# Performance work log

Measured on AMD Instinct MI355X. Metric: run time of the kernel, lower is better.

## Reference

```python
import jax, jax.numpy as jnp
import numpy as np

B, N, F, H = 1024, 64, 512, 512  # batch, n_agents, input_size, hidden


def setup_inputs() -> dict:
    key = jax.random.key(0)
    k1, k2, k3, k4, k5, k6 = jax.random.split(key, 6)
    locs = jax.random.uniform(k1, (B, N, 2), dtype=jnp.float32)
    states = jax.random.normal(k2, (B, N, F), dtype=jnp.float32)
    # CatEdgeGraphLayer: Linear(2*F + 2 -> H)
    Wg = jax.random.normal(k3, (H, 2 * F + 2), dtype=jnp.float32) / np.sqrt(2 * F + 2)
    bg = jnp.zeros((H,), dtype=jnp.float32)
    W4 = jax.random.normal(k4, (2, H), dtype=jnp.float32) / np.sqrt(H)
    b4 = jnp.zeros((2,), dtype=jnp.float32)
    W5 = jax.random.normal(k5, (1, H), dtype=jnp.float32) / np.sqrt(H)
    b5 = jnp.zeros((1,), dtype=jnp.float32)
    return {"locs": locs, "states": states, "Wg": Wg, "bg": bg,
            "W4": W4, "b4": b4, "W5": W5, "b5": b5}


def _forward(locs, states, Wg, bg, W4, b4, W5, b5):
    n = states.shape[1]
    f = states.shape[2]
    # get_diffs: pairwise position differences d[b,i,j] = locs[b,i] - locs[b,j]
    diffs = locs[:, :, None, :] - locs[:, None, :, :]          # [B,N,N,2]
    norms = jnp.linalg.norm(diffs, axis=-1)                    # [B,N,N]
    # threshold = ||normalize([1,1])|| = 1.0
    threshold = jnp.float32(1.0)
    A = (norms < threshold).astype(states.dtype)
    # normalize_adjacency: row-normalize (diagonal is 1 so rows never empty)
    A = A / jnp.sum(A, axis=-1, keepdims=True)
    # message j->i (j != i): A[b,i,j] * concat(states[b,j], diffs[b,i,j])
    Am = A * (1.0 - jnp.eye(n, dtype=A.dtype))                 # mask j == i
    # per-agent update: relu( sum_{j!=i} Linear(concat(f_i, msg_ij)) )
    # split weight by input blocks: W1 acts on f_i, W2f on f_j part, W2d on diff part
    W1, W2f, W2d = Wg[:, :f], Wg[:, f:2 * f], Wg[:, 2 * f:]
    msg_f = jnp.einsum('bij,bjf->bif', Am, states)             # sum_j A_ij f_j
    msg_d = jnp.einsum('bij,bijc->bic', Am, diffs)             # sum_j A_ij d_ij
    pre = ((n - 1) * (jnp.einsum('bif,hf->bih', states, W1) + bg)
           + jnp.einsum('bif,hf->bih', msg_f, W2f)
           + jnp.einsum('bic,hc->bih', msg_d, W2d))
    h = jax.nn.relu(pre)                                       # [B,N,H]
    policies = jnp.einsum('bih,ph->bip', h, W4) + b4           # [B,N,2]
    values = jnp.einsum('bih,vh->biv', h, W5) + b5             # [B,N,1]
    return policies, values


def reference(locs, states, Wg, bg, W4, b4, W5, b5):
    return _forward(locs, states, Wg, bg, W4, b4, W5, b5)
```

## Files before the change

### kernel.cpp

```cpp
#include <hip/hip_runtime.h>


typedef __attribute__((ext_vector_type(8))) short bf16x8;
typedef __attribute__((ext_vector_type(4))) float f32x4;
typedef __attribute__((ext_vector_type(4))) unsigned short us4;

__device__ __forceinline__ unsigned short f2bf(float x) {
  union { float f; unsigned int u; } c; c.f = x;
  return (unsigned short)((c.u + 0x7FFFu + ((c.u >> 16) & 1u)) >> 16);
}

__global__ void prep_kernel(const float* __restrict__ Wg, const float* __restrict__ bg,
                            const float* __restrict__ W4, const float* __restrict__ W5,
                            unsigned short* __restrict__ Wgb, float* __restrict__ auxw)
{
  const int h = blockIdx.x;
  const int t = threadIdx.x;
  const float* row = Wg + h * 1026;
  const int k0 = t * 4;
#pragma unroll
  for (int q = 0; q < 4; ++q) {
    int k = k0 + q;
    float s = (k < 512) ? 63.0f : 1.0f;
    Wgb[h * 1024 + k] = f2bf(s * row[k]);
  }
  if (t == 0) {
    float* a = auxw + h * 8;
    a[0] = 63.0f * bg[h];
    a[1] = row[1024];
    a[2] = row[1025];
    a[3] = W4[h];
    a[4] = W4[512 + h];
    a[5] = W5[h];
    a[6] = 0.0f; a[7] = 0.0f;
  }
}

__global__ __launch_bounds__(256, 1) void traffic_kernel(
    const float* __restrict__ locs, const float* __restrict__ states,
    const unsigned short* __restrict__ Wgb, const float* __restrict__ auxw,
    const float* __restrict__ b4, const float* __restrict__ b5,
    float* __restrict__ out)
{
  __shared__ unsigned short S[64 * 520];
  __shared__ unsigned short U2T[512 * 72];
  __shared__ unsigned short Am[64 * 72];
  __shared__ float locs_s[128];
  __shared__ float msgd[128];
  __shared__ float red[4 * 64 * 3];

  const int t = threadIdx.x;
  const int b = blockIdx.x;
  const int lane = t & 63;
  const int w = t >> 6;
  const int llo = lane & 15;
  const int lhi = lane >> 4;

  if (t < 128) locs_s[t] = locs[b * 128 + t];
  __syncthreads();

  {
    const int i = t >> 2;
    const int j0 = (t & 3) * 16;
    const float xi = locs_s[2*i], yi = locs_s[2*i+1];
    float a[16]; float psum = 0.f;
#pragma unroll
    for (int q = 0; q < 16; ++q) {
      int j = j0 + q;
      float dx = xi - locs_s[2*j];
      float dy = yi - locs_s[2*j+1];
      a[q] = (dx*dx + dy*dy < 1.0f) ? 1.0f : 0.0f;
      psum += a[q];
    }
    psum += __shfl_xor(psum, 1);
    psum += __shfl_xor(psum, 2);
    const float inv = 1.0f / psum;
    float m0 = 0.f, m1 = 0.f;
#pragma unroll
    for (int q = 0; q < 16; ++q) {
      int j = j0 + q;
      float v = (j == i) ? 0.f : a[q] * inv;
      a[q] = v;
      m0 += v * (xi - locs_s[2*j]);
      m1 += v * (yi - locs_s[2*j+1]);
    }
    m0 += __shfl_xor(m0, 1); m0 += __shfl_xor(m0, 2);
    m1 += __shfl_xor(m1, 1); m1 += __shfl_xor(m1, 2);
    if ((t & 3) == 0) { msgd[2*i] = m0; msgd[2*i+1] = m1; }
    union { unsigned short h8[8]; uint4 v4; } pk;
#pragma unroll
    for (int q = 0; q < 8; ++q) pk.h8[q] = f2bf(a[q]);
    *(uint4*)&Am[i*72 + j0] = pk.v4;
#pragma unroll
    for (int q = 0; q < 8; ++q) pk.h8[q] = f2bf(a[8+q]);
    *(uint4*)&Am[i*72 + j0 + 8] = pk.v4;
  }

  {
    const float4* sb = (const float4*)(states + (size_t)b * 32768);
#pragma unroll
    for (int it = 0; it < 32; ++it) {
      int id = it * 256 + t;
      int j = id >> 7;
      int f0 = (id & 127) * 4;
      float4 v = sb[id];
      us4 s4;
      s4.x = f2bf(v.x); s4.y = f2bf(v.y);
      s4.z = f2bf(v.z); s4.w = f2bf(v.w);
      *(us4*)&S[j * 520 + f0] = s4;
    }
  }
  __syncthreads();

  const int hw = w * 128;
  unsigned short* U2w = &U2T[w * 128 * 72];

  f32x4 acc[8][4];

  auto zero_acc = [&]() {
#pragma unroll
    for (int mt = 0; mt < 8; ++mt)
#pragma unroll
      for (int nt = 0; nt < 4; ++nt)
        acc[mt][nt] = f32x4{0.f, 0.f, 0.f, 0.f};
  };

  auto gemm_step = [&](int kg, int kl) {
    bf16x8 afr[8], bfr[4];
#pragma unroll
    for (int mt = 0; mt < 8; ++mt)
      afr[mt] = *(const bf16x8*)&Wgb[(size_t)(hw + mt*16 + llo) * 1024 + kg + lhi*8];
#pragma unroll
    for (int nt = 0; nt < 4; ++nt)
      bfr[nt] = *(const bf16x8*)&S[(nt*16 + llo) * 520 + kl + lhi*8];
#pragma unroll
    for (int mt = 0; mt < 8; ++mt)
#pragma unroll
      for (int nt = 0; nt < 4; ++nt)
        acc[mt][nt] = __builtin_amdgcn_mfma_f32_16x16x32_bf16(afr[mt], bfr[nt], acc[mt][nt], 0, 0, 0);
  };

  zero_acc();
#pragma unroll 2
  for (int ks = 0; ks < 16; ++ks) gemm_step(512 + ks*32, ks*32);

#pragma unroll
  for (int mt = 0; mt < 8; ++mt)
#pragma unroll
    for (int nt = 0; nt < 4; ++nt)
#pragma unroll
      for (int r = 0; r < 4; ++r)
        U2w[(mt*16 + lhi*4 + r) * 72 + nt*16 + llo] = f2bf(acc[mt][nt][r]);

  zero_acc();
#pragma unroll 2
  for (int ks = 0; ks < 16; ++ks) gemm_step(ks*32, ks*32);

#pragma unroll
  for (int ks = 0; ks < 2; ++ks) {
    bf16x8 afr[8], bfr[4];
#pragma unroll
    for (int mt = 0; mt < 8; ++mt)
      afr[mt] = *(const bf16x8*)&U2w[(mt*16 + llo) * 72 + ks*32 + lhi*8];
#pragma unroll
    for (int nt = 0; nt < 4; ++nt)
      bfr[nt] = *(const bf16x8*)&Am[(nt*16 + llo) * 72 + ks*32 + lhi*8];
#pragma unroll
    for (int mt = 0; mt < 8; ++mt)
#pragma unroll
      for (int nt = 0; nt < 4; ++nt)
        acc[mt][nt] = __builtin_amdgcn_mfma_f32_16x16x32_bf16(afr[mt], bfr[nt], acc[mt][nt], 0, 0, 0);
  }

  float mdx[4], mdy[4];
#pragma unroll
  for (int nt = 0; nt < 4; ++nt) {
    mdx[nt] = msgd[2*(nt*16 + llo)];
    mdy[nt] = msgd[2*(nt*16 + llo) + 1];
  }
  float pp0[4] = {0,0,0,0}, pp1[4] = {0,0,0,0}, vv[4] = {0,0,0,0};
#pragma unroll
  for (int mt = 0; mt < 8; ++mt) {
#pragma unroll
    for (int r = 0; r < 4; ++r) {
      int hh = hw + mt*16 + lhi*4 + r;
      float4 ax0 = *(const float4*)&auxw[hh*8];
      float4 ax1 = *(const float4*)&auxw[hh*8 + 4];
#pragma unroll
      for (int nt = 0; nt < 4; ++nt) {
        float val = acc[mt][nt][r] + ax0.x + mdx[nt]*ax0.y + mdy[nt]*ax0.z;
        val = fmaxf(val, 0.f);
        pp0[nt] += val * ax0.w;
        pp1[nt] += val * ax1.x;
        vv[nt]  += val * ax1.y;
      }
    }
  }
#pragma unroll
  for (int nt = 0; nt < 4; ++nt) {
    pp0[nt] += __shfl_xor(pp0[nt], 16); pp0[nt] += __shfl_xor(pp0[nt], 32);
    pp1[nt] += __shfl_xor(pp1[nt], 16); pp1[nt] += __shfl_xor(pp1[nt], 32);
    vv[nt]  += __shfl_xor(vv[nt], 16);  vv[nt]  += __shfl_xor(vv[nt], 32);
  }
  if (lane < 16) {
#pragma unroll
    for (int nt = 0; nt < 4; ++nt) {
      int i = nt*16 + llo;
      red[(w*64 + i)*3 + 0] = pp0[nt];
      red[(w*64 + i)*3 + 1] = pp1[nt];
      red[(w*64 + i)*3 + 2] = vv[nt];
    }
  }
  __syncthreads();
  if (t < 192) {
    int o = t >> 6;
    int i = t & 63;
    float s = red[(0*64+i)*3+o] + red[(1*64+i)*3+o]
            + red[(2*64+i)*3+o] + red[(3*64+i)*3+o];
    s += (o < 2) ? b4[o] : b5[0];
    if (o < 2) out[((size_t)b*64 + i)*2 + o] = s;
    else       out[(size_t)131072 + (size_t)b*64 + i] = s;
  }
}

extern "C" void kernel_launch(void* const* d_in, const int* in_sizes, int n_in,
                              void* d_out, int out_size, void* d_ws, size_t ws_size,
                              hipStream_t stream)
{
  const float* locs   = (const float*)d_in[0];
  const float* states = (const float*)d_in[1];
  const float* Wg     = (const float*)d_in[2];
  const float* bg     = (const float*)d_in[3];
  const float* W4     = (const float*)d_in[4];
  const float* b4     = (const float*)d_in[5];
  const float* W5     = (const float*)d_in[6];
  const float* b5     = (const float*)d_in[7];

  unsigned short* Wgb = (unsigned short*)d_ws;
  float* auxw = (float*)((char*)d_ws + 512 * 1024 * 2);

  prep_kernel<<<512, 256, 0, stream>>>(Wg, bg, W4, W5, Wgb, auxw);
  traffic_kernel<<<1024, 256, 0, stream>>>(locs, states, Wgb, auxw, b4, b5, (float*)d_out);
}
```

Measured before the change: 408.4 us.

## Halve LDS footprint by staging states in halves to fit two blocks per CU

The main kernel now stages the bf16 states tile in two 32-agent halves and drops the large U2T shared buffer. The W2f·S product is instead transposed through a small per-wave scratch into register A-fragments that feed the adjacency MFMA directly. This cuts shared memory enough to allow two blocks per CU (launch_bounds 256,2), aiming at better latency hiding, at the cost of an extra barrier and tighter register pressure. The prep kernel is also reshaped to write packed bf16 pairs, one pair per thread.

```diff
diff --git a/kernel.cpp b/kernel.cpp
--- a/kernel.cpp
+++ b/kernel.cpp
@@ -10,21 +10,21 @@
   return (unsigned short)((c.u + 0x7FFFu + ((c.u >> 16) & 1u)) >> 16);
 }
 
-__global__ void prep_kernel(const float* __restrict__ Wg, const float* __restrict__ bg,
-                            const float* __restrict__ W4, const float* __restrict__ W5,
-                            unsigned short* __restrict__ Wgb, float* __restrict__ auxw)
+__global__ __launch_bounds__(256) void prep_kernel(
+    const float* __restrict__ Wg, const float* __restrict__ bg,
+    const float* __restrict__ W4, const float* __restrict__ W5,
+    unsigned short* __restrict__ Wgb, float* __restrict__ auxw)
 {
-  const int h = blockIdx.x;
-  const int t = threadIdx.x;
+  const int id = blockIdx.x * 256 + threadIdx.x;
+  const int h = id >> 9;
+  const int kp = id & 511;
+  const int k = kp * 2;
   const float* row = Wg + h * 1026;
-  const int k0 = t * 4;
-#pragma unroll
-  for (int q = 0; q < 4; ++q) {
-    int k = k0 + q;
-    float s = (k < 512) ? 63.0f : 1.0f;
-    Wgb[h * 1024 + k] = f2bf(s * row[k]);
-  }
-  if (t == 0) {
+  const float s = (k < 512) ? 63.0f : 1.0f;
+  unsigned int lo = f2bf(s * row[k]);
+  unsigned int hi = f2bf(s * row[k + 1]);
+  *(unsigned int*)&Wgb[h * 1024 + k] = lo | (hi << 16);
+  if (kp == 0) {
     float* a = auxw + h * 8;
     a[0] = 63.0f * bg[h];
     a[1] = row[1024];
@@ -36,15 +36,15 @@
   }
 }
 
-__global__ __launch_bounds__(256, 1) void traffic_kernel(
+__global__ __launch_bounds__(256, 2) void traffic_kernel(
     const float* __restrict__ locs, const float* __restrict__ states,
     const unsigned short* __restrict__ Wgb, const float* __restrict__ auxw,
     const float* __restrict__ b4, const float* __restrict__ b5,
     float* __restrict__ out)
 {
-  __shared__ unsigned short S[64 * 520];
-  __shared__ unsigned short U2T[512 * 72];
+  __shared__ unsigned short S[32 * 520];
   __shared__ unsigned short Am[64 * 72];
+  __shared__ unsigned short scr[4][16 * 40];
   __shared__ float locs_s[128];
   __shared__ float msgd[128];
   __shared__ float red[4 * 64 * 3];
@@ -55,6 +55,7 @@
   const int w = t >> 6;
   const int llo = lane & 15;
   const int lhi = lane >> 4;
+  const int hw = w * 128;
 
   if (t < 128) locs_s[t] = locs[b * 128 + t];
   __syncthreads();
@@ -96,10 +97,10 @@
     *(uint4*)&Am[i*72 + j0 + 8] = pk.v4;
   }
 
-  {
-    const float4* sb = (const float4*)(states + (size_t)b * 32768);
-#pragma unroll
-    for (int it = 0; it < 32; ++it) {
+  auto stageS = [&](int half) {
+    const float4* sb = (const float4*)(states + (size_t)b * 32768 + half * 16384);
+#pragma unroll
+    for (int it = 0; it < 16; ++it) {
       int id = it * 256 + t;
       int j = id >> 7;
       int f0 = (id & 127) * 4;
@@ -109,68 +110,89 @@
       s4.z = f2bf(v.z); s4.w = f2bf(v.w);
       *(us4*)&S[j * 520 + f0] = s4;
     }
-  }
-  __syncthreads();
-
-  const int hw = w * 128;
-  unsigned short* U2w = &U2T[w * 128 * 72];
+  };
 
   f32x4 acc[8][4];
-
-  auto zero_acc = [&]() {
-#pragma unroll
-    for (int mt = 0; mt < 8; ++mt)
-#pragma unroll
-      for (int nt = 0; nt < 4; ++nt)
-        acc[mt][nt] = f32x4{0.f, 0.f, 0.f, 0.f};
-  };
-
-  auto gemm_step = [&](int kg, int kl) {
-    bf16x8 afr[8], bfr[4];
-#pragma unroll
-    for (int mt = 0; mt < 8; ++mt)
-      afr[mt] = *(const bf16x8*)&Wgb[(size_t)(hw + mt*16 + llo) * 1024 + kg + lhi*8];
-#pragma unroll
-    for (int nt = 0; nt < 4; ++nt)
-      bfr[nt] = *(const bf16x8*)&S[(nt*16 + llo) * 520 + kl + lhi*8];
-#pragma unroll
-    for (int mt = 0; mt < 8; ++mt)
-#pragma unroll
-      for (int nt = 0; nt < 4; ++nt)
-        acc[mt][nt] = __builtin_amdgcn_mfma_f32_16x16x32_bf16(afr[mt], bfr[nt], acc[mt][nt], 0, 0, 0);
-  };
-
-  zero_acc();
-#pragma unroll 2
-  for (int ks = 0; ks < 16; ++ks) gemm_step(512 + ks*32, ks*32);
-
+  bf16x8 afr_reg[8];
+  unsigned short* sc = &scr[w][0];
+  const size_t wb = (size_t)(hw + llo) * 1024 + lhi * 8;
+
+  auto c1_chunk = [&](int c) {
+    f32x4 au[4][2];
+#pragma unroll
+    for (int m = 0; m < 4; ++m)
+#pragma unroll
+      for (int n = 0; n < 2; ++n) au[m][n] = f32x4{0.f,0.f,0.f,0.f};
+#pragma unroll 4
+    for (int ks = 0; ks < 16; ++ks) {
+      bf16x8 afr[4], bfr[2];
+#pragma unroll
+      for (int m = 0; m < 4; ++m)
+        afr[m] = *(const bf16x8*)&Wgb[wb + (size_t)(c*4+m)*16384 + 512 + ks*32];
+#pragma unroll
+      for (int n = 0; n < 2; ++n)
+        bfr[n] = *(const bf16x8*)&S[(n*16 + llo)*520 + ks*32 + lhi*8];
+#pragma unroll
+      for (int m = 0; m < 4; ++m)
+#pragma unroll
+        for (int n = 0; n < 2; ++n)
+          au[m][n] = __builtin_amdgcn_mfma_f32_16x16x32_bf16(afr[m], bfr[n], au[m][n], 0, 0, 0);
+    }
+#pragma unroll
+    for (int m = 0; m < 4; ++m) {
+#pragma unroll
+      for (int n = 0; n < 2; ++n)
+#pragma unroll
+        for (int r = 0; r < 4; ++r)
+          sc[(lhi*4 + r)*40 + n*16 + llo] = f2bf(au[m][n][r]);
+      afr_reg[c*4 + m] = *(const bf16x8*)&sc[llo*40 + lhi*8];
+    }
+  };
+
+  auto dprime = [&](int half) {
+#pragma unroll
+    for (int nt = 0; nt < 4; ++nt) {
+      bf16x8 bfr = *(const bf16x8*)&Am[(nt*16 + llo)*72 + half*32 + lhi*8];
+#pragma unroll
+      for (int mt = 0; mt < 8; ++mt)
+        acc[mt][nt] = __builtin_amdgcn_mfma_f32_16x16x32_bf16(afr_reg[mt], bfr, acc[mt][nt], 0, 0, 0);
+    }
+  };
+
+  auto c2_half = [&](int half) {
+#pragma unroll 4
+    for (int ks = 0; ks < 16; ++ks) {
+      bf16x8 afr[8], bfr[2];
+#pragma unroll
+      for (int mt = 0; mt < 8; ++mt)
+        afr[mt] = *(const bf16x8*)&Wgb[wb + (size_t)mt*16384 + ks*32];
+#pragma unroll
+      for (int n = 0; n < 2; ++n)
+        bfr[n] = *(const bf16x8*)&S[(n*16 + llo)*520 + ks*32 + lhi*8];
+#pragma unroll
+      for (int mt = 0; mt < 8; ++mt)
+#pragma unroll
+        for (int n = 0; n < 2; ++n)
+          acc[mt][half*2 + n] = __builtin_amdgcn_mfma_f32_16x16x32_bf16(afr[mt], bfr[n], acc[mt][half*2 + n], 0, 0, 0);
+    }
+  };
+
+  stageS(0);
+  __syncthreads();
+  c1_chunk(0); c1_chunk(1);
 #pragma unroll
   for (int mt = 0; mt < 8; ++mt)
 #pragma unroll
-    for (int nt = 0; nt < 4; ++nt)
-#pragma unroll
-      for (int r = 0; r < 4; ++r)
-        U2w[(mt*16 + lhi*4 + r) * 72 + nt*16 + llo] = f2bf(acc[mt][nt][r]);
-
-  zero_acc();
-#pragma unroll 2
-  for (int ks = 0; ks < 16; ++ks) gemm_step(ks*32, ks*32);
-
-#pragma unroll
-  for (int ks = 0; ks < 2; ++ks) {
-    bf16x8 afr[8], bfr[4];
-#pragma unroll
-    for (int mt = 0; mt < 8; ++mt)
-      afr[mt] = *(const bf16x8*)&U2w[(mt*16 + llo) * 72 + ks*32 + lhi*8];
-#pragma unroll
-    for (int nt = 0; nt < 4; ++nt)
-      bfr[nt] = *(const bf16x8*)&Am[(nt*16 + llo) * 72 + ks*32 + lhi*8];
-#pragma unroll
-    for (int mt = 0; mt < 8; ++mt)
-#pragma unroll
-      for (int nt = 0; nt < 4; ++nt)
-        acc[mt][nt] = __builtin_amdgcn_mfma_f32_16x16x32_bf16(afr[mt], bfr[nt], acc[mt][nt], 0, 0, 0);
-  }
+    for (int nt = 0; nt < 4; ++nt) acc[mt][nt] = f32x4{0.f,0.f,0.f,0.f};
+  dprime(0);
+  c2_half(0);
+  __syncthreads();
+
+  stageS(1);
+  __syncthreads();
+  c1_chunk(0); c1_chunk(1);
+  dprime(1);
+  c2_half(1);
 
   float mdx[4], mdy[4];
 #pragma unroll
@@ -239,6 +261,6 @@
   unsigned short* Wgb = (unsigned short*)d_ws;
   float* auxw = (float*)((char*)d_ws + 512 * 1024 * 2);
 
-  prep_kernel<<<512, 256, 0, stream>>>(Wg, bg, W4, W5, Wgb, auxw);
+  prep_kernel<<<1024, 256, 0, stream>>>(Wg, bg, W4, W5, Wgb, auxw);
   traffic_kernel<<<1024, 256, 0, stream>>>(locs, states, Wgb, auxw, b4, b5, (float*)d_out);
 }
```

New measurement: 455.6 us. +11.5%, slower.
